# Optimization experiments

Measured on AMD Instinct MI355X. Metric: run time of the kernel, lower is better.

The kernel has to match this reference:

```python
import jax, jax.numpy as jnp
import numpy as np

N, E, G = 50000, 800000, 64
IN, H, ED, OUT = 32, 96, 16, 128
EPS_GEN = 1e-7   # GENConv message eps
EPS_BN = 1e-5    # BatchNorm1d eps


def _bn(x, g, b):
    # training-mode BatchNorm1d: batch stats, biased variance
    mu = jnp.mean(x, axis=0)
    var = jnp.var(x, axis=0)
    return (x - mu) * jax.lax.rsqrt(var + EPS_BN) * g + b


def _genconv(x_src, x_dst, src, dst, ea, mw1, mg, mb, mw2):
    # message: relu(x_j + e_ij) + eps            [E, H]
    msg = jax.nn.relu(x_src[src] + ea) + EPS_GEN
    n = x_dst.shape[0]
    # softmax aggregation over incoming edges per dst node (t=1.0)
    m = jax.ops.segment_max(msg, dst, num_segments=n)
    ex = jnp.exp(msg - m[dst])
    s = jax.ops.segment_sum(ex, dst, num_segments=n)
    agg = jax.ops.segment_sum(msg * (ex / s[dst]), dst, num_segments=n)
    h = agg + x_dst
    # GENConv internal MLP: Lin(H,2H,no bias) -> BN -> ReLU -> Lin(2H,H,no bias)
    h = jax.nn.relu(_bn(h @ mw1, mg, mb))
    return h @ mw2


def _forward(x, edge_attr, w_src1, w_dst1, w_edge1,
             mlp1_w1, mlp1_g, mlp1_b, mlp1_w2, bn1_g, bn1_b,
             w_edge2, mlp2_w1, mlp2_g, mlp2_b, mlp2_w2, bn2_g, bn2_b,
             w_edge3, mlp3_w1, mlp3_g, mlp3_b, mlp3_w2, bn3_g, bn3_b,
             lin_w, lin_b, edge_index, batch):
    src, dst = edge_index[0], edge_index[1]
    h = _genconv(x @ w_src1, x @ w_dst1, src, dst, edge_attr @ w_edge1,
                 mlp1_w1, mlp1_g, mlp1_b, mlp1_w2)
    h = jax.nn.relu(_bn(h, bn1_g, bn1_b))
    h = _genconv(h, h, src, dst, edge_attr @ w_edge2,
                 mlp2_w1, mlp2_g, mlp2_b, mlp2_w2)
    h = jax.nn.relu(_bn(h, bn2_g, bn2_b))
    h = _genconv(h, h, src, dst, edge_attr @ w_edge3,
                 mlp3_w1, mlp3_g, mlp3_b, mlp3_w2)
    h = jax.nn.relu(_bn(h, bn3_g, bn3_b))
    # global mean pool over graphs (dropout is identity in eval)
    cnt = jax.ops.segment_sum(jnp.ones((h.shape[0],), h.dtype), batch, num_segments=G)
    pooled = jax.ops.segment_sum(h, batch, num_segments=G) / jnp.maximum(cnt, 1.0)[:, None]
    return pooled @ lin_w + lin_b


def setup_inputs() -> dict:
    key = jax.random.key(0)
    ks = jax.random.split(key, 20)
    rn = lambda i, shp, s=0.05: jax.random.normal(ks[i], shp, jnp.float32) * s
    return {
        'x': rn(0, (N, IN), 1.0),
        'edge_attr': rn(1, (E, ED), 1.0),
        'edge_index': jax.random.randint(ks[2], (2, E), 0, N, jnp.int32),
        'batch': jnp.sort(jax.random.randint(ks[3], (N,), 0, G, jnp.int32)),
        'w_src1': rn(4, (IN, H)), 'w_dst1': rn(5, (IN, H)), 'w_edge1': rn(6, (ED, H)),
        'mlp1_w1': rn(7, (H, 2 * H)), 'mlp1_g': jnp.ones(2 * H), 'mlp1_b': jnp.zeros(2 * H),
        'mlp1_w2': rn(8, (2 * H, H)), 'bn1_g': jnp.ones(H), 'bn1_b': jnp.zeros(H),
        'w_edge2': rn(9, (ED, H)),
        'mlp2_w1': rn(10, (H, 2 * H)), 'mlp2_g': jnp.ones(2 * H), 'mlp2_b': jnp.zeros(2 * H),
        'mlp2_w2': rn(11, (2 * H, H)), 'bn2_g': jnp.ones(H), 'bn2_b': jnp.zeros(H),
        'w_edge3': rn(12, (ED, H)),
        'mlp3_w1': rn(13, (H, 2 * H)), 'mlp3_g': jnp.ones(2 * H), 'mlp3_b': jnp.zeros(2 * H),
        'mlp3_w2': rn(14, (2 * H, H)), 'bn3_g': jnp.ones(H), 'bn3_b': jnp.zeros(H),
        'lin_w': rn(15, (H, OUT)), 'lin_b': jnp.zeros(OUT),
    }


def reference(x, edge_attr, edge_index, batch, w_src1, w_dst1, w_edge1,
              mlp1_w1, mlp1_g, mlp1_b, mlp1_w2, bn1_g, bn1_b,
              w_edge2, mlp2_w1, mlp2_g, mlp2_b, mlp2_w2, bn2_g, bn2_b,
              w_edge3, mlp3_w1, mlp3_g, mlp3_b, mlp3_w2, bn3_g, bn3_b,
              lin_w, lin_b):
    return _forward(x, edge_attr, w_src1, w_dst1, w_edge1,
                    mlp1_w1, mlp1_g, mlp1_b, mlp1_w2, bn1_g, bn1_b,
                    w_edge2, mlp2_w1, mlp2_g, mlp2_b, mlp2_w2, bn2_g, bn2_b,
                    w_edge3, mlp3_w1, mlp3_g, mlp3_b, mlp3_w2, bn3_g, bn3_b,
                    lin_w, lin_b, edge_index, batch)
```

## Files before the change

### kernel.cpp

```cpp
#include <hip/hip_runtime.h>
#include <math.h>

#define NN 50000
#define EE 800000
#define GG 64
#define HH 96
#define H2 192
#define INF 32
#define EDF 16
#define OUTF 128
#define EPS_GEN 1e-7f
#define EPS_BN 1e-5f
#define NPB 100
#define NB_SCAN 49
#define NBH (256 * NB_SCAN)
#define BSCAN_PT 13
#define LOG2E 1.44269504088896f
#define SHIFT2 28.85390081777927f
#define GRIDP 512
#define NT64 ((NN + 63) / 64)
#define PROJ_GRID 1024
#define WPREP_N (4608 + 6 * 18432)

typedef _Float16 f16;
typedef _Float16 f16x2 __attribute__((ext_vector_type(2)));
typedef _Float16 f16x8 __attribute__((ext_vector_type(8)));
typedef float f32x4 __attribute__((ext_vector_type(4)));

static inline size_t align256(size_t x) { return (x + 255) & ~(size_t)255; }

__device__ __forceinline__ float fdot2(f16x2 a, f16x2 b, float c) {
#if __has_builtin(__builtin_amdgcn_fdot2)
    return __builtin_amdgcn_fdot2(a, b, c, false);
#else
    return fmaf((float)a.x, (float)b.x, fmaf((float)a.y, (float)b.y, c));
#endif
}

__device__ __forceinline__ float exp2fast(float x) {
#if __has_builtin(__builtin_amdgcn_exp2f)
    return __builtin_amdgcn_exp2f(x);
#else
    return exp2f(x);
#endif
}

union W8 { float4 f[2]; f16x2 h[8]; };
union EAu { float4 f; f16x2 h[4]; };
union XUu { float2 f; f16x2 h[2]; };

__device__ __forceinline__ void agg_step(const EAu& e0, const EAu& e1, const XUu& xu,
                                         const W8* w, float* num, float* den) {
    float xv[4] = {(float)xu.h[0].x, (float)xu.h[0].y, (float)xu.h[1].x, (float)xu.h[1].y};
    #pragma unroll
    for (int cc = 0; cc < 4; ++cc) {
        float acc = 0.f;
        #pragma unroll
        for (int k = 0; k < 4; ++k) acc = fdot2(e0.h[k], w[cc].h[k], acc);
        #pragma unroll
        for (int k = 0; k < 4; ++k) acc = fdot2(e1.h[k], w[cc].h[4 + k], acc);
        float msg = fmaxf(xv[cc] + acc, 0.f) + EPS_GEN;
        float p = exp2fast(fmaf(msg, LOG2E, -SHIFT2));
        den[cc] += p;
        num[cc] = fmaf(msg, p, num[cc]);
    }
}


__global__ __launch_bounds__(256) void hist_kernel(const int* __restrict__ dst,
                                                   int* __restrict__ deg,
                                                   int* __restrict__ rank) {
    int e = blockIdx.x * 256 + threadIdx.x;
    if (e >= EE) return;
    rank[e] = atomicAdd(&deg[dst[e]], 1);
}

__global__ __launch_bounds__(1024) void scan1_kernel(const int* __restrict__ deg,
                                                     int* __restrict__ offs,
                                                     int* __restrict__ bsum,
                                                     int* __restrict__ bhist) {
    __shared__ int ws[16];
    __shared__ int lh[256];
    int tid = threadIdx.x, lane = tid & 63, w = tid >> 6;
    if (tid < 256) lh[tid] = 0;
    int i = blockIdx.x * 1024 + tid;
    int v = (i < NN) ? deg[i] : 0;
    __syncthreads();
    if (i < NN) {
        int b = 255 - (v > 255 ? 255 : v);
        atomicAdd(&lh[b], 1);
    }
    int x = v;
    #pragma unroll
    for (int off = 1; off < 64; off <<= 1) {
        int y = __shfl_up(x, off, 64);
        if (lane >= off) x += y;
    }
    if (lane == 63) ws[w] = x;
    __syncthreads();
    int wpre = 0;
    for (int j = 0; j < w; ++j) wpre += ws[j];
    if (i < NN) offs[i] = wpre + x - v;
    if (tid == 1023) bsum[blockIdx.x] = wpre + x;
    if (tid < 256) bhist[tid * NB_SCAN + blockIdx.x] = lh[tid];
}

__global__ __launch_bounds__(1024) void bscan_kernel(int* __restrict__ bhist,
                                                     int* __restrict__ bsum,
                                                     float* __restrict__ pool) {
    __shared__ int ws[16];
    int tid = threadIdx.x, lane = tid & 63, w = tid >> 6;
    for (int i = tid; i < GG * HH; i += 1024) pool[i] = 0.f;
    if (tid < 64) {
        int v = (tid < NB_SCAN) ? bsum[tid] : 0;
        int x = v;
        #pragma unroll
        for (int off = 1; off < 64; off <<= 1) {
            int y = __shfl_up(x, off, 64);
            if (lane >= off) x += y;
        }
        if (tid < NB_SCAN) bsum[tid] = x - v;
    }
    int base = tid * BSCAN_PT;
    int loc[BSCAN_PT];
    int s = 0;
    #pragma unroll
    for (int i = 0; i < BSCAN_PT; ++i) {
        int idx = base + i;
        int v = (idx < NBH) ? bhist[idx] : 0;
        loc[i] = s;
        s += v;
    }
    int x = s;
    #pragma unroll
    for (int off = 1; off < 64; off <<= 1) {
        int y = __shfl_up(x, off, 64);
        if (lane >= off) x += y;
    }
    if (lane == 63) ws[w] = x;
    __syncthreads();
    int wpre = 0;
    for (int j = 0; j < w; ++j) wpre += ws[j];
    int pre = wpre + x - s;
    #pragma unroll
    for (int i = 0; i < BSCAN_PT; ++i) {
        int idx = base + i;
        if (idx < NBH) bhist[idx] = pre + loc[i];
    }
}

__global__ __launch_bounds__(1024) void finsort_kernel(int* __restrict__ offs,
                                                       const int* __restrict__ bsum,
                                                       const int* __restrict__ deg,
                                                       const int* __restrict__ bhist,
                                                       int* __restrict__ perm) {
    __shared__ int cnt[256];
    int tid = threadIdx.x;
    if (tid < 256) cnt[tid] = 0;
    __syncthreads();
    int n = blockIdx.x * 1024 + tid;
    if (n < NN) {
        offs[n] += bsum[blockIdx.x];
        int d = deg[n];
        int b = 255 - (d > 255 ? 255 : d);
        int rank = atomicAdd(&cnt[b], 1);
        perm[bhist[b * NB_SCAN + blockIdx.x] + rank] = n;
    }
    if (n == NN) offs[NN] = EE;
}

__global__ __launch_bounds__(256) void scatter_kernel(const int* __restrict__ src,
                                                      const int* __restrict__ dst,
                                                      const int* __restrict__ offs,
                                                      const int* __restrict__ rank,
                                                      const float* __restrict__ eattr,
                                                      int* __restrict__ csr_src,
                                                      float4* __restrict__ csrea) {
    int e = blockIdx.x * 256 + threadIdx.x;
    if (e >= EE) return;
    int d = dst[e];
    int slot = offs[d] + rank[e];
    csr_src[slot] = src[e] * (HH * 2);
    const float4* ep = (const float4*)(eattr + (size_t)e * EDF);
    float4 v0 = ep[0], v1 = ep[1], v2 = ep[2], v3 = ep[3];
    union { f16x2 h[4]; float4 f; } a, b;
    a.h[0] = f16x2{(f16)v0.x, (f16)v0.y};
    a.h[1] = f16x2{(f16)v0.z, (f16)v0.w};
    a.h[2] = f16x2{(f16)v1.x, (f16)v1.y};
    a.h[3] = f16x2{(f16)v1.z, (f16)v1.w};
    b.h[0] = f16x2{(f16)v2.x, (f16)v2.y};
    b.h[1] = f16x2{(f16)v2.z, (f16)v2.w};
    b.h[2] = f16x2{(f16)v3.x, (f16)v3.y};
    b.h[3] = f16x2{(f16)v3.z, (f16)v3.w};
    float4* outp = csrea + (size_t)slot * 4;
    outp[0] = a.f;
    outp[1] = b.f;
    outp[2] = float4{0.f, 0.f, 0.f, 0.f};
    outp[3] = float4{0.f, 0.f, 0.f, 0.f};
}


__global__ __launch_bounds__(256) void proj_kernel(
    const float* __restrict__ x, const float* __restrict__ ws, const float* __restrict__ wd,
    const float* __restrict__ we0, const float* __restrict__ we1, const float* __restrict__ we2,
    const float* __restrict__ m10, const float* __restrict__ m11, const float* __restrict__ m12,
    const float* __restrict__ m20, const float* __restrict__ m21, const float* __restrict__ m22,
    f16* __restrict__ wte, f16* __restrict__ wt1, f16* __restrict__ wt2,
    int* __restrict__ csr_src, f16* __restrict__ xs, f16* __restrict__ xd) {
    __shared__ float Ws[INF * HH], Wd[INF * HH];
    int tid = threadIdx.x;
    int idx = blockIdx.x * 256 + tid;
    if (idx < 8) csr_src[EE + idx] = 0;
    if (idx < 4608) {
        const float* w = (idx < 1536) ? we0 : ((idx < 3072) ? we1 : we2);
        int r = idx % 1536, c = r / EDF, k = r % EDF;
        wte[idx] = (f16)w[k * HH + c];
    } else if (idx < 4608 + 3 * 18432) {
        int m = idx - 4608;
        const float* w = (m < 18432) ? m10 : ((m < 36864) ? m11 : m12);
        int r = m % 18432, j = r / HH, k = r % HH;
        wt1[m] = (f16)w[k * H2 + j];
    } else if (idx < WPREP_N) {
        int m = idx - 4608 - 3 * 18432;
        const float* w = (m < 18432) ? m20 : ((m < 36864) ? m21 : m22);
        int r = m % 18432, j = r / H2, k = r % H2;
        wt2[m] = (f16)w[k * HH + j];
    }
    for (int i = tid; i < INF * HH; i += 256) { Ws[i] = ws[i]; Wd[i] = wd[i]; }
    __syncthreads();
    for (int gid = blockIdx.x * 256 + tid; gid < NN * HH; gid += PROJ_GRID * 256) {
        int n = gid / HH, c = gid % HH;
        const float* xr = x + (size_t)n * INF;
        float as = 0.f, ad = 0.f;
        #pragma unroll
        for (int k = 0; k < INF; ++k) {
            float xv = xr[k];
            as = fmaf(xv, Ws[k * HH + c], as);
            ad = fmaf(xv, Wd[k * HH + c], ad);
        }
        xs[gid] = (f16)as;
        xd[gid] = (f16)ad;
    }
}


#define AGG_LOAD(E0, E1, XU, JJ, SO)                                     \
    E0.f = csrea[(size_t)(JJ) * 4];                                      \
    E1.f = csrea[(size_t)(JJ) * 4 + 1];                                  \
    XU.f = *(const float2*)(xsrcb + (size_t)(unsigned)(SO) + c0 * 2);

__global__ __launch_bounds__(192) void agg_kernel(const f16* __restrict__ xsrc,
                                                  const f16* __restrict__ xdst,
                                                  const float4* __restrict__ csrea,
                                                  const f16* __restrict__ wt,
                                                  const int* __restrict__ offs,
                                                  const int* __restrict__ csr_src,
                                                  const int* __restrict__ perm,
                                                  float* __restrict__ stats,
                                                  f16* __restrict__ hpre) {
    int tid = threadIdx.x;
    if (blockIdx.x == 0) {
        for (int t = tid; t < 576; t += 192) stats[t] = 0.f;
    }
    int idx = blockIdx.x * 8 + tid / 24;
    if (idx >= NN) return;
    int node = perm[idx];
    int cg = tid % 24, c0 = cg * 4;
    const char* xsrcb = (const char*)xsrc;
    W8 w[4];
    #pragma unroll
    for (int cc = 0; cc < 4; ++cc) {
        const float4* wp = (const float4*)(wt + (c0 + cc) * EDF);
        w[cc].f[0] = wp[0];
        w[cc].f[1] = wp[1];
    }
    XUu xd;
    xd.f = *(const float2*)(xdst + (size_t)node * HH + c0);
    int s0 = offs[node], s1 = offs[node + 1];
    float num[4] = {0.f, 0.f, 0.f, 0.f}, den[4] = {0.f, 0.f, 0.f, 0.f};
    if (s0 < s1) {
        int last = s1 - 1;
        EAu eA0, eA1, eB0, eB1, eC0, eC1;
        XUu xA, xB, xC;
        int sA = csr_src[s0], sB = csr_src[s0 + 1], sC = csr_src[s0 + 2];
        AGG_LOAD(eA0, eA1, xA, s0, sA)
        AGG_LOAD(eB0, eB1, xB, s0 + 1, sB)
        AGG_LOAD(eC0, eC1, xC, s0 + 2, sC)
        int sD = csr_src[s0 + 3], sE = csr_src[s0 + 4], sF = csr_src[s0 + 5];
        for (int j = s0; j < s1; j += 3) {
            __builtin_amdgcn_s_setprio(1);
            agg_step(eA0, eA1, xA, w, num, den);
            __builtin_amdgcn_s_setprio(0);
            AGG_LOAD(eA0, eA1, xA, j + 3, sD)
            sD = csr_src[j + 6];
            if (j + 1 <= last) {
                __builtin_amdgcn_s_setprio(1);
                agg_step(eB0, eB1, xB, w, num, den);
                __builtin_amdgcn_s_setprio(0);
            }
            AGG_LOAD(eB0, eB1, xB, j + 4, sE)
            sE = csr_src[j + 7];
            if (j + 2 <= last) {
                __builtin_amdgcn_s_setprio(1);
                agg_step(eC0, eC1, xC, w, num, den);
                __builtin_amdgcn_s_setprio(0);
            }
            AGG_LOAD(eC0, eC1, xC, j + 5, sF)
            sF = csr_src[j + 8];
        }
    }
    float xdv[4] = {(float)xd.h[0].x, (float)xd.h[0].y, (float)xd.h[1].x, (float)xd.h[1].y};
    float r0 = (den[0] > 0.f) ? num[0] / den[0] : 0.f;
    float r1 = (den[1] > 0.f) ? num[1] / den[1] : 0.f;
    float r2 = (den[2] > 0.f) ? num[2] / den[2] : 0.f;
    float r3 = (den[3] > 0.f) ? num[3] / den[3] : 0.f;
    union { float2 f; f16x2 h[2]; } o;
    o.h[0] = f16x2{(f16)(r0 + xdv[0]), (f16)(r1 + xdv[1])};
    o.h[1] = f16x2{(f16)(r2 + xdv[2]), (f16)(r3 + xdv[3])};
    *(float2*)(hpre + (size_t)node * HH + c0) = o.f;
}

#define LDA1 104

__global__ __launch_bounds__(256) void gemm1_kernel(const f16* __restrict__ A,
                                                    const f16* __restrict__ Wt,
                                                    f16* __restrict__ T,
                                                    float* __restrict__ colsum,
                                                    float* __restrict__ colsumsq) {
    __shared__ f16 Al[64 * LDA1];
    __shared__ f16 Wl[192 * LDA1];
    __shared__ float red[H2 * 2];
    int tid = threadIdx.x;
    for (int v = tid; v < 192 * 12; v += 256) {
        int r = v / 12, c8 = (v % 12) * 8;
        *(float4*)(Wl + r * LDA1 + c8) = *(const float4*)(Wt + r * HH + c8);
    }
    for (int t = tid; t < H2 * 2; t += 256) red[t] = 0.f;
    __syncthreads();
    int wv = tid >> 6, l = tid & 63, lr = l & 15, lg = l >> 4;
    int i0 = wv * 16;
    float sa[12], qa[12];
    #pragma unroll
    for (int t = 0; t < 12; ++t) { sa[t] = 0.f; qa[t] = 0.f; }
    for (int tile = blockIdx.x; tile < NT64; tile += GRIDP) {
        int n0 = tile * 64;
        for (int v = tid; v < 64 * 12; v += 256) {
            int r = v / 12, c8 = (v % 12) * 8;
            float4 d = {0.f, 0.f, 0.f, 0.f};
            if (n0 + r < NN) d = *(const float4*)(A + (size_t)(n0 + r) * HH + c8);
            *(float4*)(Al + r * LDA1 + c8) = d;
        }
        __syncthreads();
        f32x4 acc[12];
        #pragma unroll
        for (int t = 0; t < 12; ++t) acc[t] = (f32x4){0.f, 0.f, 0.f, 0.f};
        #pragma unroll
        for (int ks = 0; ks < 3; ++ks) {
            int k0 = ks * 32 + lg * 8;
            f16x8 af = *(const f16x8*)(Al + (i0 + lr) * LDA1 + k0);
            #pragma unroll
            for (int t = 0; t < 12; ++t) {
                f16x8 bf = *(const f16x8*)(Wl + (t * 16 + lr) * LDA1 + k0);
                acc[t] = __builtin_amdgcn_mfma_f32_16x16x32_f16(af, bf, acc[t], 0, 0, 0);
            }
        }
        #pragma unroll
        for (int t = 0; t < 12; ++t) {
            int col = t * 16 + lr;
            #pragma unroll
            for (int rr = 0; rr < 4; ++rr) {
                int row = n0 + i0 + lg * 4 + rr;
                float v = acc[t][rr];
                if (row < NN) {
                    T[(size_t)row * H2 + col] = (f16)v;
                    sa[t] += v;
                    qa[t] = fmaf(v, v, qa[t]);
                }
            }
        }
        __syncthreads();
    }
    #pragma unroll
    for (int t = 0; t < 12; ++t) {
        float s = sa[t], q = qa[t];
        s += __shfl_xor(s, 16); s += __shfl_xor(s, 32);
        q += __shfl_xor(q, 16); q += __shfl_xor(q, 32);
        if (lg == 0) { atomicAdd(&red[t * 16 + lr], s); atomicAdd(&red[H2 + t * 16 + lr], q); }
    }
    __syncthreads();
    if (tid < H2) {
        atomicAdd(&colsum[tid], red[tid]);
        atomicAdd(&colsumsq[tid], red[H2 + tid]);
    }
}

#define LDA2 200

__global__ __launch_bounds__(256) void gemm2_kernel(const f16* __restrict__ T,
                                                    const f16* __restrict__ Wt,
                                                    const float* __restrict__ cs1,
                                                    const float* __restrict__ cq1,
                                                    const float* __restrict__ g1,
                                                    const float* __restrict__ b1,
                                                    f16* __restrict__ U,
                                                    float* __restrict__ colsum,
                                                    float* __restrict__ colsumsq) {
    __shared__ f16 Al[64 * LDA2];
    __shared__ f16 Wl[96 * LDA2];
    __shared__ float ab[H2 * 2];
    __shared__ float red[HH * 2];
    int tid = threadIdx.x;
    if (tid < H2) {
        const float invN = 1.f / (float)NN;
        float mu = cs1[tid] * invN;
        float var = fmaxf(cq1[tid] * invN - mu * mu, 0.f);
        float a = g1[tid] * rsqrtf(var + EPS_BN);
        ab[tid] = a;
        ab[H2 + tid] = b1[tid] - mu * a;
    }
    if (tid < HH * 2) red[tid] = 0.f;
    for (int v = tid; v < 96 * 24; v += 256) {
        int r = v / 24, c8 = (v % 24) * 8;
        *(float4*)(Wl + r * LDA2 + c8) = *(const float4*)(Wt + r * H2 + c8);
    }
    __syncthreads();
    int wv = tid >> 6, l = tid & 63, lr = l & 15, lg = l >> 4;
    int i0 = wv * 16;
    float sa[6], qa[6];
    #pragma unroll
    for (int t = 0; t < 6; ++t) { sa[t] = 0.f; qa[t] = 0.f; }
    for (int tile = blockIdx.x; tile < NT64; tile += GRIDP) {
        int n0 = tile * 64;
        for (int v = tid; v < 64 * 24; v += 256) {
            int r = v / 24, c8 = (v % 24) * 8;
            float4 dd = {0.f, 0.f, 0.f, 0.f};
            if (n0 + r < NN) {
                union { float4 f; f16x2 h[4]; } u, o;
                u.f = *(const float4*)(T + (size_t)(n0 + r) * H2 + c8);
                #pragma unroll
                for (int p = 0; p < 4; ++p) {
                    float x0 = fmaxf(fmaf((float)u.h[p].x, ab[c8 + 2 * p], ab[H2 + c8 + 2 * p]), 0.f);
                    float x1 = fmaxf(fmaf((float)u.h[p].y, ab[c8 + 2 * p + 1], ab[H2 + c8 + 2 * p + 1]), 0.f);
                    o.h[p] = f16x2{(f16)x0, (f16)x1};
                }
                dd = o.f;
            }
            *(float4*)(Al + r * LDA2 + c8) = dd;
        }
        __syncthreads();
        f32x4 acc[6];
        #pragma unroll
        for (int t = 0; t < 6; ++t) acc[t] = (f32x4){0.f, 0.f, 0.f, 0.f};
        #pragma unroll
        for (int ks = 0; ks < 6; ++ks) {
            int k0 = ks * 32 + lg * 8;
            f16x8 af = *(const f16x8*)(Al + (i0 + lr) * LDA2 + k0);
            #pragma unroll
            for (int t = 0; t < 6; ++t) {
                f16x8 bf = *(const f16x8*)(Wl + (t * 16 + lr) * LDA2 + k0);
                acc[t] = __builtin_amdgcn_mfma_f32_16x16x32_f16(af, bf, acc[t], 0, 0, 0);
            }
        }
        #pragma unroll
        for (int t = 0; t < 6; ++t) {
            int col = t * 16 + lr;
            #pragma unroll
            for (int rr = 0; rr < 4; ++rr) {
                int row = n0 + i0 + lg * 4 + rr;
                float v = acc[t][rr];
                if (row < NN) {
                    U[(size_t)row * HH + col] = (f16)v;
                    sa[t] += v;
                    qa[t] = fmaf(v, v, qa[t]);
                }
            }
        }
        __syncthreads();
    }
    #pragma unroll
    for (int t = 0; t < 6; ++t) {
        float s = sa[t], q = qa[t];
        s += __shfl_xor(s, 16); s += __shfl_xor(s, 32);
        q += __shfl_xor(q, 16); q += __shfl_xor(q, 32);
        if (lg == 0) { atomicAdd(&red[t * 16 + lr], s); atomicAdd(&red[HH + t * 16 + lr], q); }
    }
    __syncthreads();
    if (tid < HH) {
        atomicAdd(&colsum[tid], red[tid]);
        atomicAdd(&colsumsq[tid], red[HH + tid]);
    }
}


__global__ __launch_bounds__(256) void elem_kernel(const f16* __restrict__ U,
                                                   const float* __restrict__ cs2,
                                                   const float* __restrict__ cq2,
                                                   const float* __restrict__ g2,
                                                   const float* __restrict__ b2,
                                                   f16* __restrict__ Hout) {
    __shared__ float ab[HH * 2];
    int tid = threadIdx.x;
    if (tid < HH) {
        const float invN = 1.f / (float)NN;
        float mu = cs2[tid] * invN;
        float var = fmaxf(cq2[tid] * invN - mu * mu, 0.f);
        float a = g2[tid] * rsqrtf(var + EPS_BN);
        ab[tid] = a;
        ab[HH + tid] = b2[tid] - mu * a;
    }
    __syncthreads();
    int i = blockIdx.x * 256 + tid;
    if (i >= NN * HH / 8) return;
    union { float4 f; f16x2 h[4]; } u, o;
    u.f = ((const float4*)U)[i];
    int k = (i % 12) * 8;
    #pragma unroll
    for (int p = 0; p < 4; ++p) {
        float x0 = fmaxf(fmaf((float)u.h[p].x, ab[k + 2 * p], ab[HH + k + 2 * p]), 0.f);
        float x1 = fmaxf(fmaf((float)u.h[p].y, ab[k + 2 * p + 1], ab[HH + k + 2 * p + 1]), 0.f);
        o.h[p] = f16x2{(f16)x0, (f16)x1};
    }
    ((float4*)Hout)[i] = o.f;
}


__global__ __launch_bounds__(192) void pool_bn_kernel(const f16* __restrict__ U,
                                                      const float* __restrict__ cs2,
                                                      const float* __restrict__ cq2,
                                                      const float* __restrict__ g2,
                                                      const float* __restrict__ b2,
                                                      const int* __restrict__ batch,
                                                      float* __restrict__ pool) {
    __shared__ float ab[HH * 2];
    int tid = threadIdx.x;
    if (tid < HH) {
        const float invN = 1.f / (float)NN;
        float mu = cs2[tid] * invN;
        float var = fmaxf(cq2[tid] * invN - mu * mu, 0.f);
        float a = g2[tid] * rsqrtf(var + EPS_BN);
        ab[tid] = a;
        ab[HH + tid] = b2[tid] - mu * a;
    }
    __syncthreads();
    int n0 = blockIdx.x * NPB;
    int n1 = (n0 + NPB < NN) ? n0 + NPB : NN;
    int c = tid % HH;
    int h = tid / HH;
    float a_ = ab[c], b_ = ab[HH + c];
    float acc = 0.f;
    int gcur = -1;
    for (int n = n0 + h; n < n1; n += 2) {
        int g = batch[n];
        if (g != gcur) {
            if (gcur >= 0) atomicAdd(&pool[gcur * HH + c], acc);
            acc = 0.f;
            gcur = g;
        }
        acc += fmaxf(fmaf((float)U[(size_t)n * HH + c], a_, b_), 0.f);
    }
    if (gcur >= 0) atomicAdd(&pool[gcur * HH + c], acc);
}

__global__ __launch_bounds__(128) void out_kernel(const float* __restrict__ pool,
                                                  const int* __restrict__ batch,
                                                  const float* __restrict__ lw,
                                                  const float* __restrict__ lb,
                                                  float* __restrict__ out) {
    int g = blockIdx.x, o = threadIdx.x;
    int lo = 0, hi = NN;
    while (lo < hi) { int mid = (lo + hi) >> 1; if (batch[mid] < g) lo = mid + 1; else hi = mid; }
    int s = lo;
    lo = 0; hi = NN;
    while (lo < hi) { int mid = (lo + hi) >> 1; if (batch[mid] < g + 1) lo = mid + 1; else hi = mid; }
    float inv = 1.f / fmaxf((float)(lo - s), 1.f);
    float acc = lb[o];
    for (int c = 0; c < HH; ++c) acc = fmaf(pool[g * HH + c] * inv, lw[c * OUTF + o], acc);
    out[(size_t)g * OUTF + o] = acc;
}


extern "C" void kernel_launch(void* const* d_in, const int* in_sizes, int n_in,
                              void* d_out, int out_size, void* d_ws, size_t ws_size,
                              hipStream_t stream) {
    const float* x = (const float*)d_in[0];
    const float* eattr = (const float*)d_in[1];
    const int* eidx = (const int*)d_in[2];
    const int* batch = (const int*)d_in[3];
    const float* w_src1 = (const float*)d_in[4];
    const float* w_dst1 = (const float*)d_in[5];
    const float* w_e[3] = {(const float*)d_in[6], (const float*)d_in[13], (const float*)d_in[20]};
    const float* mw1[3] = {(const float*)d_in[7], (const float*)d_in[14], (const float*)d_in[21]};
    const float* mg[3] = {(const float*)d_in[8], (const float*)d_in[15], (const float*)d_in[22]};
    const float* mb[3] = {(const float*)d_in[9], (const float*)d_in[16], (const float*)d_in[23]};
    const float* mw2[3] = {(const float*)d_in[10], (const float*)d_in[17], (const float*)d_in[24]};
    const float* bng[3] = {(const float*)d_in[11], (const float*)d_in[18], (const float*)d_in[25]};
    const float* bnb[3] = {(const float*)d_in[12], (const float*)d_in[19], (const float*)d_in[26]};
    const float* lin_w = (const float*)d_in[27];
    const float* lin_b = (const float*)d_in[28];
    float* out = (float*)d_out;

    const int* src = eidx;
    const int* dst = eidx + EE;

    char* base = (char*)d_ws;
    size_t off = 0;
    int* deg = (int*)(base + off); off = align256(off + (size_t)NN * 4);
    int* offs = (int*)(base + off); off = align256(off + (size_t)(NN + 1) * 4);
    int* bsum = (int*)(base + off); off = align256(off + (size_t)NB_SCAN * 4);
    int* bhist = (int*)(base + off); off = align256(off + (size_t)NBH * 4);
    int* perm = (int*)(base + off); off = align256(off + (size_t)NN * 4);
    int* csr_src = (int*)(base + off); off = align256(off + (size_t)(EE + 8) * 4);
    float* stats = (float*)(base + off); off = align256(off + 576 * 4);
    float* colsum1 = stats;
    float* colsumsq1 = stats + 192;
    float* colsum2 = stats + 384;
    float* colsumsq2 = stats + 480;
    float* pool = (float*)(base + off); off = align256(off + (size_t)GG * HH * 4);
    f16* wte = (f16*)(base + off); off = align256(off + (size_t)3 * 1536 * 2);
    f16* wt1 = (f16*)(base + off); off = align256(off + (size_t)3 * 18432 * 2);
    f16* wt2 = (f16*)(base + off); off = align256(off + (size_t)3 * 18432 * 2);
    f16* XS = (f16*)(base + off); off = align256(off + (size_t)NN * HH * 2);
    f16* XD = (f16*)(base + off); off = align256(off + (size_t)NN * HH * 2);
    f16* HP = (f16*)(base + off); off = align256(off + (size_t)NN * HH * 2);
    f16* T = (f16*)(base + off); off = align256(off + (size_t)NN * H2 * 2);
    float4* csrea = (float4*)(base + off); off = align256(off + (size_t)(EE + 8) * 64);
    int* rank = (int*)T;
    (void)in_sizes; (void)n_in; (void)out_size; (void)ws_size;

    hipMemsetAsync(deg, 0, (size_t)NN * 4, stream);
    hist_kernel<<<(EE + 255) / 256, 256, 0, stream>>>(dst, deg, rank);
    scan1_kernel<<<NB_SCAN, 1024, 0, stream>>>(deg, offs, bsum, bhist);
    bscan_kernel<<<1, 1024, 0, stream>>>(bhist, bsum, pool);
    finsort_kernel<<<NB_SCAN, 1024, 0, stream>>>(offs, bsum, deg, bhist, perm);
    scatter_kernel<<<(EE + 255) / 256, 256, 0, stream>>>(src, dst, offs, rank, eattr,
                                                         csr_src, csrea);
    proj_kernel<<<PROJ_GRID, 256, 0, stream>>>(
        x, w_src1, w_dst1, w_e[0], w_e[1], w_e[2], mw1[0], mw1[1], mw1[2],
        mw2[0], mw2[1], mw2[2], wte, wt1, wt2, csr_src, XS, XD);

    for (int l = 0; l < 3; ++l) {
        const f16* xdst = (l == 0) ? XD : XS;
        agg_kernel<<<(NN + 7) / 8, 192, 0, stream>>>(XS, xdst, csrea, wte + l * 1536, offs,
                                                     csr_src, perm, stats, HP);
        gemm1_kernel<<<GRIDP, 256, 0, stream>>>(HP, wt1 + l * 18432, T, colsum1, colsumsq1);
        gemm2_kernel<<<GRIDP, 256, 0, stream>>>(T, wt2 + l * 18432, colsum1, colsumsq1,
                                                mg[l], mb[l], HP, colsum2, colsumsq2);
        if (l < 2)
            elem_kernel<<<(NN * HH / 8 + 255) / 256, 256, 0, stream>>>(HP, colsum2, colsumsq2,
                                                                       bng[l], bnb[l], XS);
    }

    pool_bn_kernel<<<(NN + NPB - 1) / NPB, 192, 0, stream>>>(HP, colsum2, colsumsq2,
                                                             bng[2], bnb[2], batch, pool);
    out_kernel<<<GG, 128, 0, stream>>>(pool, batch, lin_w, lin_b, out);
}
```

Measured before the change: 485.8 us.

## Split each node's edge list across two lanes in aggregation kernel

The aggregation kernel now assigns 48 threads per node instead of 24, with lane pairs interleaving even and odd edges and combining partial softmax numerators and denominators via a lane shuffle. This doubles thread-level parallelism and memory-level parallelism for the per-node gather, cutting the serial edge-loop length. The CSR padding is enlarged and the padded edge-attribute slots are zeroed so prefetches past the end stay in bounds. In exchange, the grid is doubled, redundant weight loads per thread increase, and a shuffle reduction is added.

```diff
diff --git a/kernel.cpp b/kernel.cpp
--- a/kernel.cpp
+++ b/kernel.cpp
@@ -21,6 +21,7 @@
 #define NT64 ((NN + 63) / 64)
 #define PROJ_GRID 1024
 #define WPREP_N (4608 + 6 * 18432)
+#define CSRPAD 16
 
 typedef _Float16 f16;
 typedef _Float16 f16x2 __attribute__((ext_vector_type(2)));
@@ -206,11 +207,16 @@
     const float* __restrict__ m10, const float* __restrict__ m11, const float* __restrict__ m12,
     const float* __restrict__ m20, const float* __restrict__ m21, const float* __restrict__ m22,
     f16* __restrict__ wte, f16* __restrict__ wt1, f16* __restrict__ wt2,
-    int* __restrict__ csr_src, f16* __restrict__ xs, f16* __restrict__ xd) {
+    int* __restrict__ csr_src, float4* __restrict__ csrea,
+    f16* __restrict__ xs, f16* __restrict__ xd) {
     __shared__ float Ws[INF * HH], Wd[INF * HH];
     int tid = threadIdx.x;
     int idx = blockIdx.x * 256 + tid;
-    if (idx < 8) csr_src[EE + idx] = 0;
+    if (idx < CSRPAD) {
+        csr_src[EE + idx] = 0;
+        csrea[(size_t)(EE + idx) * 4] = float4{0.f, 0.f, 0.f, 0.f};
+        csrea[(size_t)(EE + idx) * 4 + 1] = float4{0.f, 0.f, 0.f, 0.f};
+    }
     if (idx < 4608) {
         const float* w = (idx < 1536) ? we0 : ((idx < 3072) ? we1 : we2);
         int r = idx % 1536, c = r / EDF, k = r % EDF;
@@ -262,10 +268,11 @@
     if (blockIdx.x == 0) {
         for (int t = tid; t < 576; t += 192) stats[t] = 0.f;
     }
-    int idx = blockIdx.x * 8 + tid / 24;
+    int idx = blockIdx.x * 4 + tid / 48;
     if (idx >= NN) return;
     int node = perm[idx];
-    int cg = tid % 24, c0 = cg * 4;
+    int half = tid & 1;
+    int cg = (tid % 48) >> 1, c0 = cg * 4;
     const char* xsrcb = (const char*)xsrc;
     W8 w[4];
     #pragma unroll
@@ -274,50 +281,57 @@
         w[cc].f[0] = wp[0];
         w[cc].f[1] = wp[1];
     }
-    XUu xd;
-    xd.f = *(const float2*)(xdst + (size_t)node * HH + c0);
     int s0 = offs[node], s1 = offs[node + 1];
     float num[4] = {0.f, 0.f, 0.f, 0.f}, den[4] = {0.f, 0.f, 0.f, 0.f};
-    if (s0 < s1) {
-        int last = s1 - 1;
+    int jh = s0 + half;
+    if (jh < s1) {
         EAu eA0, eA1, eB0, eB1, eC0, eC1;
         XUu xA, xB, xC;
-        int sA = csr_src[s0], sB = csr_src[s0 + 1], sC = csr_src[s0 + 2];
-        AGG_LOAD(eA0, eA1, xA, s0, sA)
-        AGG_LOAD(eB0, eB1, xB, s0 + 1, sB)
-        AGG_LOAD(eC0, eC1, xC, s0 + 2, sC)
-        int sD = csr_src[s0 + 3], sE = csr_src[s0 + 4], sF = csr_src[s0 + 5];
-        for (int j = s0; j < s1; j += 3) {
+        int sA = csr_src[jh], sB = csr_src[jh + 2], sC = csr_src[jh + 4];
+        AGG_LOAD(eA0, eA1, xA, jh, sA)
+        AGG_LOAD(eB0, eB1, xB, jh + 2, sB)
+        AGG_LOAD(eC0, eC1, xC, jh + 4, sC)
+        int sD = csr_src[jh + 6], sE = csr_src[jh + 8], sF = csr_src[jh + 10];
+        for (int j = jh; j < s1; j += 6) {
             __builtin_amdgcn_s_setprio(1);
             agg_step(eA0, eA1, xA, w, num, den);
             __builtin_amdgcn_s_setprio(0);
-            AGG_LOAD(eA0, eA1, xA, j + 3, sD)
-            sD = csr_src[j + 6];
-            if (j + 1 <= last) {
+            AGG_LOAD(eA0, eA1, xA, j + 6, sD)
+            sD = csr_src[j + 12];
+            if (j + 2 < s1) {
                 __builtin_amdgcn_s_setprio(1);
                 agg_step(eB0, eB1, xB, w, num, den);
                 __builtin_amdgcn_s_setprio(0);
             }
-            AGG_LOAD(eB0, eB1, xB, j + 4, sE)
-            sE = csr_src[j + 7];
-            if (j + 2 <= last) {
+            AGG_LOAD(eB0, eB1, xB, j + 8, sE)
+            sE = csr_src[j + 14];
+            if (j + 4 < s1) {
                 __builtin_amdgcn_s_setprio(1);
                 agg_step(eC0, eC1, xC, w, num, den);
                 __builtin_amdgcn_s_setprio(0);
             }
-            AGG_LOAD(eC0, eC1, xC, j + 5, sF)
-            sF = csr_src[j + 8];
-        }
-    }
-    float xdv[4] = {(float)xd.h[0].x, (float)xd.h[0].y, (float)xd.h[1].x, (float)xd.h[1].y};
-    float r0 = (den[0] > 0.f) ? num[0] / den[0] : 0.f;
-    float r1 = (den[1] > 0.f) ? num[1] / den[1] : 0.f;
-    float r2 = (den[2] > 0.f) ? num[2] / den[2] : 0.f;
-    float r3 = (den[3] > 0.f) ? num[3] / den[3] : 0.f;
-    union { float2 f; f16x2 h[2]; } o;
-    o.h[0] = f16x2{(f16)(r0 + xdv[0]), (f16)(r1 + xdv[1])};
-    o.h[1] = f16x2{(f16)(r2 + xdv[2]), (f16)(r3 + xdv[3])};
-    *(float2*)(hpre + (size_t)node * HH + c0) = o.f;
+            AGG_LOAD(eC0, eC1, xC, j + 10, sF)
+            sF = csr_src[j + 16];
+        }
+    }
+    #pragma unroll
+    for (int cc = 0; cc < 4; ++cc) {
+        num[cc] += __shfl_xor(num[cc], 1);
+        den[cc] += __shfl_xor(den[cc], 1);
+    }
+    if (half == 0) {
+        XUu xd;
+        xd.f = *(const float2*)(xdst + (size_t)node * HH + c0);
+        float xdv[4] = {(float)xd.h[0].x, (float)xd.h[0].y, (float)xd.h[1].x, (float)xd.h[1].y};
+        float r0 = (den[0] > 0.f) ? num[0] / den[0] : 0.f;
+        float r1 = (den[1] > 0.f) ? num[1] / den[1] : 0.f;
+        float r2 = (den[2] > 0.f) ? num[2] / den[2] : 0.f;
+        float r3 = (den[3] > 0.f) ? num[3] / den[3] : 0.f;
+        union { float2 f; f16x2 h[2]; } o;
+        o.h[0] = f16x2{(f16)(r0 + xdv[0]), (f16)(r1 + xdv[1])};
+        o.h[1] = f16x2{(f16)(r2 + xdv[2]), (f16)(r3 + xdv[3])};
+        *(float2*)(hpre + (size_t)node * HH + c0) = o.f;
+    }
 }
 
 #define LDA1 104
@@ -609,7 +623,7 @@
     int* bsum = (int*)(base + off); off = align256(off + (size_t)NB_SCAN * 4);
     int* bhist = (int*)(base + off); off = align256(off + (size_t)NBH * 4);
     int* perm = (int*)(base + off); off = align256(off + (size_t)NN * 4);
-    int* csr_src = (int*)(base + off); off = align256(off + (size_t)(EE + 8) * 4);
+    int* csr_src = (int*)(base + off); off = align256(off + (size_t)(EE + CSRPAD) * 4);
     float* stats = (float*)(base + off); off = align256(off + 576 * 4);
     float* colsum1 = stats;
     float* colsumsq1 = stats + 192;
@@ -623,7 +637,7 @@
     f16* XD = (f16*)(base + off); off = align256(off + (size_t)NN * HH * 2);
     f16* HP = (f16*)(base + off); off = align256(off + (size_t)NN * HH * 2);
     f16* T = (f16*)(base + off); off = align256(off + (size_t)NN * H2 * 2);
-    float4* csrea = (float4*)(base + off); off = align256(off + (size_t)(EE + 8) * 64);
+    float4* csrea = (float4*)(base + off); off = align256(off + (size_t)(EE + CSRPAD) * 64);
     int* rank = (int*)T;
     (void)in_sizes; (void)n_in; (void)out_size; (void)ws_size;
 
@@ -636,11 +650,11 @@
                                                          csr_src, csrea);
     proj_kernel<<<PROJ_GRID, 256, 0, stream>>>(
         x, w_src1, w_dst1, w_e[0], w_e[1], w_e[2], mw1[0], mw1[1], mw1[2],
-        mw2[0], mw2[1], mw2[2], wte, wt1, wt2, csr_src, XS, XD);
+        mw2[0], mw2[1], mw2[2], wte, wt1, wt2, csr_src, csrea, XS, XD);
 
     for (int l = 0; l < 3; ++l) {
         const f16* xdst = (l == 0) ? XD : XS;
-        agg_kernel<<<(NN + 7) / 8, 192, 0, stream>>>(XS, xdst, csrea, wte + l * 1536, offs,
+        agg_kernel<<<(NN + 3) / 4, 192, 0, stream>>>(XS, xdst, csrea, wte + l * 1536, offs,
                                                      csr_src, perm, stats, HP);
         gemm1_kernel<<<GRIDP, 256, 0, stream>>>(HP, wt1 + l * 18432, T, colsum1, colsumsq1);
         gemm2_kernel<<<GRIDP, 256, 0, stream>>>(T, wt2 + l * 18432, colsum1, colsumsq1,
```

Measured after the change: 518.7 us. +6.8%, slower.
